# Kernel optimization log

Measured on AMD Instinct MI355X. Metric: run time of the kernel, lower is better.

The kernel has to match this reference:

```python
import jax, jax.numpy as jnp
import numpy as np

EMB = 1024
N_HEAD = 16
D_QK = 128  # emb_dim // h_qk
D_V = 128   # emb_dim // h_v


def setup_inputs() -> dict:
    key = jax.random.key(0)
    ks = jax.random.split(key, 9)
    s_in = 1.0 / np.sqrt(EMB)
    s_pr = 1.0 / np.sqrt(N_HEAD * D_V)
    return {
        "X": jax.random.normal(ks[0], (2, 2048, EMB), dtype=jnp.float32),
        "Wq": jax.random.uniform(ks[1], (EMB, N_HEAD * D_QK), jnp.float32, -s_in, s_in),
        "bq": jax.random.uniform(ks[2], (N_HEAD * D_QK,), jnp.float32, -s_in, s_in),
        "Wk": jax.random.uniform(ks[3], (EMB, N_HEAD * D_QK), jnp.float32, -s_in, s_in),
        "bk": jax.random.uniform(ks[4], (N_HEAD * D_QK,), jnp.float32, -s_in, s_in),
        "Wv": jax.random.uniform(ks[5], (EMB, N_HEAD * D_V), jnp.float32, -s_in, s_in),
        "bv": jax.random.uniform(ks[6], (N_HEAD * D_V,), jnp.float32, -s_in, s_in),
        "Wp": jax.random.uniform(ks[7], (N_HEAD * D_V, EMB), jnp.float32, -s_pr, s_pr),
        "bp": jax.random.uniform(ks[8], (EMB,), jnp.float32, -s_pr, s_pr),
    }


def reference(X, Wq, bq, Wk, bk, Wv, bv, Wp, bp):
    b, t, d = X.shape
    # projections -> (b, h, t, dh)
    Q = (X @ Wq + bq).reshape(b, t, N_HEAD, D_QK).transpose(0, 2, 1, 3)
    K = (X @ Wk + bk).reshape(b, t, N_HEAD, D_QK).transpose(0, 2, 1, 3)
    V = (X @ Wv + bv).reshape(b, t, N_HEAD, D_V).transpose(0, 2, 1, 3)
    scale = 1.0 / jnp.sqrt(jnp.asarray(D_QK, X.dtype))
    att = jnp.einsum("bhqd,bhkd->bhqk", Q, K) * scale  # (b,h,t,t)
    causal = jnp.tril(jnp.ones((t, t), dtype=bool))
    att = jnp.where(causal[None, None], att, jnp.asarray(-jnp.inf, att.dtype))
    att = jax.nn.softmax(att, axis=-1)
    y = jnp.einsum("bhqk,bhkd->bhqd", att, V)
    y = y.transpose(0, 2, 1, 3).reshape(b, t, N_HEAD * D_V)
    return y @ Wp + bp
```

## Files before the change

kernel.cpp:

```cpp
#include <hip/hip_runtime.h>
#include <hip/hip_bf16.h>
#include <math.h>

#define EMB   1024
#define NHEAD 16
#define DHEAD 128
#define TSEQ  2048
#define NB    2
#define MROWS (NB * TSEQ)
#define QKVN  (NHEAD * DHEAD)

typedef __bf16 bf16x8 __attribute__((ext_vector_type(8)));
typedef __bf16 bf16x4 __attribute__((ext_vector_type(4)));
typedef float  f32x4  __attribute__((ext_vector_type(4)));

__device__ __forceinline__ unsigned pk_bf16(float a, float b) {
  union { __bf16 h; unsigned short u; } ca, cb;
  ca.h = (__bf16)a; cb.h = (__bf16)b;
  return (unsigned)ca.u | ((unsigned)cb.u << 16);
}

__global__ __launch_bounds__(256) void prep(
    const float* __restrict__ X,
    const float* __restrict__ Wq, const float* __restrict__ Wk,
    const float* __restrict__ Wv, const float* __restrict__ Wp,
    __bf16* __restrict__ Xb, __bf16* __restrict__ Wqt, __bf16* __restrict__ Wkt,
    __bf16* __restrict__ Wvt, __bf16* __restrict__ Wpt) {
  const int z = blockIdx.z;
  if (z == 4) {
    size_t id = ((size_t)(blockIdx.y * 64 + blockIdx.x)) * 2048 + threadIdx.x * 8;
    float4 v0 = *(const float4*)(X + id);
    float4 v1 = *(const float4*)(X + id + 4);
    bf16x8 o = {(__bf16)v0.x, (__bf16)v0.y, (__bf16)v0.z, (__bf16)v0.w,
                (__bf16)v1.x, (__bf16)v1.y, (__bf16)v1.z, (__bf16)v1.w};
    *(bf16x8*)(Xb + id) = o;
    return;
  }
  __shared__ __bf16 tile[32][33];
  const float* in; __bf16* out; int K_, N_, k0, n0;
  if (z < 3) {
    in = z == 0 ? Wq : z == 1 ? Wk : Wv;
    out = z == 0 ? Wqt : z == 1 ? Wkt : Wvt;
    K_ = EMB; N_ = QKVN; k0 = blockIdx.y * 32; n0 = blockIdx.x * 32;
  } else {
    in = Wp; out = Wpt; K_ = QKVN; N_ = EMB; k0 = blockIdx.x * 32; n0 = blockIdx.y * 32;
  }
  const int c = threadIdx.x & 31, r = threadIdx.x >> 5;
#pragma unroll
  for (int i = 0; i < 4; ++i) {
    int kk = r + i * 8;
    tile[kk][c] = (__bf16)in[(size_t)(k0 + kk) * N_ + n0 + c];
  }
  __syncthreads();
#pragma unroll
  for (int i = 0; i < 4; ++i) {
    int nn = r + i * 8;
    out[(size_t)(n0 + nn) * K_ + k0 + c] = tile[c][nn];
  }
}

template <int TM, int MODE, typename OT>
__device__ __forceinline__ void gemm_core(
    const __bf16* __restrict__ A, const __bf16* __restrict__ Bt,
    const float* __restrict__ bias, OT* __restrict__ C,
    int N, int K, int brow, int bcol, float osc,
    __bf16* As, __bf16* Bs) {
  const int tid = threadIdx.x;
  const int wv = tid >> 6, ln = tid & 63;
  const int cl = ln & 15, gp = ln >> 4;
  constexpr int SJ = (TM == 128) ? 4 : 2;
  const int rbase = (TM == 128) ? (wv >> 1) * 64 : 0;
  const int cbase = (TM == 128) ? (wv & 1) * 64 : wv * 32;

  f32x4 acc[4][SJ];
#pragma unroll
  for (int i = 0; i < 4; ++i)
#pragma unroll
    for (int j = 0; j < SJ; ++j) acc[i][j] = (f32x4){0.f, 0.f, 0.f, 0.f};

  for (int k0 = 0; k0 < K; k0 += 64) {
#pragma unroll
    for (int i = 0; i < TM / 32; ++i) {
      int idx = i * 256 + tid;
      int r = idx >> 3, cp = idx & 7, c = cp ^ (r & 7);
      __builtin_amdgcn_global_load_lds(
          (const __attribute__((address_space(1))) unsigned int*)(A + (size_t)(brow + r) * K + k0 + c * 8),
          (__attribute__((address_space(3))) unsigned int*)(As + (size_t)(i * 256 + wv * 64) * 8),
          16, 0, 0);
    }
#pragma unroll
    for (int i = 0; i < 4; ++i) {
      int idx = i * 256 + tid;
      int r = idx >> 3, cp = idx & 7, c = cp ^ (r & 7);
      __builtin_amdgcn_global_load_lds(
          (const __attribute__((address_space(1))) unsigned int*)(Bt + (size_t)(bcol + r) * K + k0 + c * 8),
          (__attribute__((address_space(3))) unsigned int*)(Bs + (size_t)(i * 256 + wv * 64) * 8),
          16, 0, 0);
    }
    __syncthreads();

#pragma unroll
    for (int kc = 0; kc < 2; ++kc) {
      bf16x8 af[4], bfr[SJ];
#pragma unroll
      for (int i = 0; i < 4; ++i) {
        int r = rbase + i * 16 + cl;
        int c = kc * 4 + gp;
        af[i] = *(const bf16x8*)(As + ((size_t)(r * 8 + (c ^ (r & 7)))) * 8);
      }
#pragma unroll
      for (int j = 0; j < SJ; ++j) {
        int r = cbase + j * 16 + cl;
        int c = kc * 4 + gp;
        bfr[j] = *(const bf16x8*)(Bs + ((size_t)(r * 8 + (c ^ (r & 7)))) * 8);
      }
#pragma unroll
      for (int i = 0; i < 4; ++i)
#pragma unroll
        for (int j = 0; j < SJ; ++j)
          acc[i][j] = __builtin_amdgcn_mfma_f32_16x16x32_bf16(af[i], bfr[j], acc[i][j], 0, 0, 0);
    }
    __syncthreads();
  }

#pragma unroll
  for (int j = 0; j < SJ; ++j) {
    int col = bcol + cbase + j * 16 + cl;
    float bb = bias[col];
    int h = col >> 7, d = col & 127;
#pragma unroll
    for (int i = 0; i < 4; ++i) {
      int row0 = brow + rbase + i * 16 + gp * 4;
#pragma unroll
      for (int rr = 0; rr < 4; ++rr) {
        float val = (acc[i][j][rr] + bb) * osc;
        if constexpr (MODE == 3) {
          C[(size_t)(row0 + rr) * N + col] = val;
        } else {
          int row = row0 + rr;
          int b = row >> 11, tok = row & 2047;
          int bh = b * NHEAD + h;
          size_t idx;
          if constexpr (MODE == 0) {
            idx = (((size_t)bh * 64 + (tok >> 5)) * 8 + ((tok >> 4) & 1) * 4 + (d >> 5)) * 512
                + (((d >> 3) & 3) * 16 + (tok & 15)) * 8 + (d & 7);
          } else if constexpr (MODE == 1) {
            idx = (((size_t)bh * 32 + (tok >> 6)) * 16 + ((tok >> 4) & 3) * 4 + (d >> 5)) * 512
                + (((d >> 3) & 3) * 16 + (tok & 15)) * 8 + (d & 7);
          } else {
            idx = (((size_t)bh * 32 + (tok >> 6)) * 16 + (d >> 4) * 2 + ((tok >> 5) & 1)) * 512
                + (((tok >> 3) & 3) * 16 + (d & 15)) * 8 + (tok & 7);
          }
          ((__bf16*)C)[idx] = (__bf16)val;
        }
      }
    }
  }
}

__global__ __launch_bounds__(256) void gemm_qkv(
    const __bf16* __restrict__ A,
    const __bf16* __restrict__ Wqt, const __bf16* __restrict__ Wkt, const __bf16* __restrict__ Wvt,
    const float* __restrict__ bq, const float* __restrict__ bk, const float* __restrict__ bv,
    __bf16* __restrict__ Qblk, __bf16* __restrict__ Kblk, __bf16* __restrict__ Vblk) {
  __shared__ __bf16 As[8192], Bs[8192];
  const int z = blockIdx.z;
  if (z == 0) {
    gemm_core<128, 0, __bf16>(A, Wqt, bq, Qblk, QKVN, EMB, blockIdx.y * 128, blockIdx.x * 128,
                              0.08838834764831845f, As, Bs);
  } else if (z == 1) {
    gemm_core<128, 1, __bf16>(A, Wkt, bk, Kblk, QKVN, EMB, blockIdx.y * 128, blockIdx.x * 128,
                              1.0f, As, Bs);
  } else {
    gemm_core<128, 2, __bf16>(A, Wvt, bv, Vblk, QKVN, EMB, blockIdx.y * 128, blockIdx.x * 128,
                              1.0f, As, Bs);
  }
}

__global__ __launch_bounds__(256) void gemm_proj(
    const __bf16* __restrict__ A, const __bf16* __restrict__ Bt,
    const float* __restrict__ bias, float* __restrict__ C) {
  __shared__ __bf16 As[4096], Bs[8192];
  gemm_core<64, 3, float>(A, Bt, bias, C, EMB, QKVN, blockIdx.y * 64, blockIdx.x * 128,
                          1.0f, As, Bs);
}

__global__ __launch_bounds__(64) void attn_mfma(
    const __bf16* __restrict__ Qblk, const __bf16* __restrict__ Kblk,
    const __bf16* __restrict__ Vblk, __bf16* __restrict__ Y) {
  const int ln = threadIdx.x;
  const int cl = ln & 15, gp = ln >> 4;

  const int x = blockIdx.x;
  const int bh = x & 31;
  const int qt = 63 - (x >> 5);
  const int b = bh >> 4, h = bh & 15;
  const int ntiles = (qt >> 1) + 1;
  const int qloc = qt * 32;
  const size_t grow = (size_t)b * TSEQ + qloc;

  bf16x8 qa[2][4];
  const __bf16* qb = Qblk + (((size_t)bh * 64 + qt) * 8) * 512 + ln * 8;
#pragma unroll
  for (int i = 0; i < 2; ++i)
#pragma unroll
    for (int kc = 0; kc < 4; ++kc)
      qa[i][kc] = *(const bf16x8*)(qb + (i * 4 + kc) * 512);

  f32x4 o[2][8];
#pragma unroll
  for (int i = 0; i < 2; ++i)
#pragma unroll
    for (int n = 0; n < 8; ++n) o[i][n] = (f32x4){0.f, 0.f, 0.f, 0.f};
  float l[2] = {0.f, 0.f};

  const int m0 = 32 * (gp & 1) + cl;
  const int m1 = m0 + 16;
  const bool hi = gp >= 2;

  for (int kt = 0; kt < ntiles; ++kt) {
    const __bf16* kb = Kblk + (((size_t)bh * 32 + kt) * 16) * 512 + ln * 8;
    const __bf16* vb = Vblk + (((size_t)bh * 32 + kt) * 16) * 512 + ln * 8;

    f32x4 sacc[2][4];
#pragma unroll
    for (int i = 0; i < 2; ++i)
#pragma unroll
      for (int s = 0; s < 4; ++s) sacc[i][s] = (f32x4){0.f, 0.f, 0.f, 0.f};
#pragma unroll
    for (int s = 0; s < 4; ++s) {
      bf16x8 kfr[4];
#pragma unroll
      for (int kc = 0; kc < 4; ++kc)
        kfr[kc] = *(const bf16x8*)(kb + (s * 4 + kc) * 512);
#pragma unroll
      for (int kc = 0; kc < 4; ++kc) {
        sacc[0][s] = __builtin_amdgcn_mfma_f32_16x16x32_bf16(kfr[kc], qa[0][kc], sacc[0][s], 0, 0, 0);
        sacc[1][s] = __builtin_amdgcn_mfma_f32_16x16x32_bf16(kfr[kc], qa[1][kc], sacc[1][s], 0, 0, 0);
      }
    }
    const bool diag = (kt * 64 + 63 > qloc);
    unsigned pk[2][4][2];
#pragma unroll
    for (int i = 0; i < 2; ++i) {
      float psum = 0.f;
      int q = qloc + i * 16 + cl;
#pragma unroll
      for (int s = 0; s < 4; ++s) {
        float e[4];
#pragma unroll
        for (int rg = 0; rg < 4; ++rg) {
          e[rg] = __expf(sacc[i][s][rg]);
          if (diag && (kt * 64 + s * 16 + gp * 4 + rg) > q) e[rg] = 0.f;
          psum += e[rg];
        }
        pk[i][s][0] = pk_bf16(e[0], e[1]);
        pk[i][s][1] = pk_bf16(e[2], e[3]);
      }
      psum += __shfl_xor(psum, 16, 64);
      psum += __shfl_xor(psum, 32, 64);
      l[i] += psum;
    }
#pragma unroll
    for (int k2 = 0; k2 < 2; ++k2) {
      bf16x8 vfr[8];
#pragma unroll
      for (int ds = 0; ds < 8; ++ds)
        vfr[ds] = *(const bf16x8*)(vb + (ds * 2 + k2) * 512);
      union PU { unsigned u[4]; bf16x8 v; } pf[2];
#pragma unroll
      for (int i = 0; i < 2; ++i) {
        unsigned a0 = __shfl(pk[i][2 * k2][0], m0, 64);
        unsigned b0 = __shfl(pk[i][2 * k2 + 1][0], m0, 64);
        unsigned a1 = __shfl(pk[i][2 * k2][1], m0, 64);
        unsigned b1 = __shfl(pk[i][2 * k2 + 1][1], m0, 64);
        unsigned a2 = __shfl(pk[i][2 * k2][0], m1, 64);
        unsigned b2 = __shfl(pk[i][2 * k2 + 1][0], m1, 64);
        unsigned a3 = __shfl(pk[i][2 * k2][1], m1, 64);
        unsigned b3 = __shfl(pk[i][2 * k2 + 1][1], m1, 64);
        pf[i].u[0] = hi ? b0 : a0;
        pf[i].u[1] = hi ? b1 : a1;
        pf[i].u[2] = hi ? b2 : a2;
        pf[i].u[3] = hi ? b3 : a3;
      }
#pragma unroll
      for (int ds = 0; ds < 8; ++ds) {
        o[0][ds] = __builtin_amdgcn_mfma_f32_16x16x32_bf16(vfr[ds], pf[0].v, o[0][ds], 0, 0, 0);
        o[1][ds] = __builtin_amdgcn_mfma_f32_16x16x32_bf16(vfr[ds], pf[1].v, o[1][ds], 0, 0, 0);
      }
    }
  }

#pragma unroll
  for (int i = 0; i < 2; ++i) {
    float inv = 1.0f / l[i];
    __bf16* yrow = Y + (grow + i * 16 + cl) * QKVN + h * DHEAD;
#pragma unroll
    for (int ds = 0; ds < 8; ++ds) {
      bf16x4 st = {(__bf16)(o[i][ds][0] * inv), (__bf16)(o[i][ds][1] * inv),
                   (__bf16)(o[i][ds][2] * inv), (__bf16)(o[i][ds][3] * inv)};
      *(bf16x4*)(yrow + ds * 16 + gp * 4) = st;
    }
  }
}

extern "C" void kernel_launch(void* const* d_in, const int* in_sizes, int n_in,
                              void* d_out, int out_size, void* d_ws, size_t ws_size,
                              hipStream_t stream) {
  const float* X  = (const float*)d_in[0];
  const float* Wq = (const float*)d_in[1];
  const float* bq = (const float*)d_in[2];
  const float* Wk = (const float*)d_in[3];
  const float* bk = (const float*)d_in[4];
  const float* Wv = (const float*)d_in[5];
  const float* bv = (const float*)d_in[6];
  const float* Wp = (const float*)d_in[7];
  const float* bp = (const float*)d_in[8];
  float* out = (float*)d_out;

  const size_t xsz = (size_t)MROWS * EMB;
  const size_t wsz = (size_t)EMB * QKVN;
  const size_t msz = (size_t)MROWS * QKVN;
  __bf16* Xb   = (__bf16*)d_ws;
  __bf16* Wqt  = Xb + xsz;
  __bf16* Wkt  = Wqt + wsz;
  __bf16* Wvt  = Wkt + wsz;
  __bf16* Wpt  = Wvt + wsz;
  __bf16* Qblk = Wpt + wsz;
  __bf16* Kblk = Qblk + msz;
  __bf16* Vblk = Kblk + msz;
  __bf16* Yb   = Vblk + msz;

  dim3 blk(256);

  prep<<<dim3(64, 32, 5), blk, 0, stream>>>(X, Wq, Wk, Wv, Wp, Xb, Wqt, Wkt, Wvt, Wpt);

  gemm_qkv<<<dim3(QKVN / 128, MROWS / 128, 3), blk, 0, stream>>>(
      Xb, Wqt, Wkt, Wvt, bq, bk, bv, Qblk, Kblk, Vblk);

  attn_mfma<<<dim3(2048), dim3(64), 0, stream>>>(Qblk, Kblk, Vblk, Yb);

  gemm_proj<<<dim3(EMB / 128, MROWS / 64), blk, 0, stream>>>(Yb, Wpt, bp, out);
}
```

Measured before the change: 303.4 us.

## Split long causal attention rows across KV chunks with atomic fp32 accumulation

Query tiles with long causal KV ranges are split into chunks of up to 8 KV tiles, so 5120 single-wave blocks run instead of 2048 with uneven work. Partial unnormalised outputs and row sums are accumulated with fp32 atomics into a zeroed workspace. A new kernel then normalises them and writes bf16 Y; short rows still write Y directly. This trades the original load imbalance and tail for a large memset, heavy atomic traffic and an extra kernel launch. It is only correct if the partial softmax uses a shared fixed offset rather than a per-block running max.

Measured after the change: 481.9 us. 58.8% more time.

```diff
diff --git a/kernel.cpp b/kernel.cpp
--- a/kernel.cpp
+++ b/kernel.cpp
@@ -185,19 +185,27 @@
                           1.0f, As, Bs);
 }
 
-__global__ __launch_bounds__(64) void attn_mfma(
+__global__ __launch_bounds__(64) void attn_part(
     const __bf16* __restrict__ Qblk, const __bf16* __restrict__ Kblk,
-    const __bf16* __restrict__ Vblk, __bf16* __restrict__ Y) {
+    const __bf16* __restrict__ Vblk, __bf16* __restrict__ Y,
+    float* __restrict__ Oacc, float* __restrict__ Lacc) {
   const int ln = threadIdx.x;
   const int cl = ln & 15, gp = ln >> 4;
 
   const int x = blockIdx.x;
   const int bh = x & 31;
-  const int qt = 63 - (x >> 5);
+  const int w = x >> 5;
+  int qt, c;
+  if (w < 64)       { qt = 48 + (w >> 2); c = w & 3; }
+  else if (w < 112) { int u = w - 64; int q3 = u / 3; qt = 32 + q3; c = u - 3 * q3; }
+  else if (w < 144) { int u = w - 112; qt = 16 + (u >> 1); c = u & 1; }
+  else              { qt = w - 144; c = 0; }
+  const int nt = (qt >> 1) + 1;
+  const int t0 = c * 8;
+  const int t1 = (t0 + 8 < nt) ? (t0 + 8) : nt;
+
   const int b = bh >> 4, h = bh & 15;
-  const int ntiles = (qt >> 1) + 1;
   const int qloc = qt * 32;
-  const size_t grow = (size_t)b * TSEQ + qloc;
 
   bf16x8 qa[2][4];
   const __bf16* qb = Qblk + (((size_t)bh * 64 + qt) * 8) * 512 + ln * 8;
@@ -218,7 +226,7 @@
   const int m1 = m0 + 16;
   const bool hi = gp >= 2;
 
-  for (int kt = 0; kt < ntiles; ++kt) {
+  for (int kt = t0; kt < t1; ++kt) {
     const __bf16* kb = Kblk + (((size_t)bh * 32 + kt) * 16) * 512 + ln * 8;
     const __bf16* vb = Vblk + (((size_t)bh * 32 + kt) * 16) * 512 + ln * 8;
 
@@ -291,16 +299,58 @@
     }
   }
 
-#pragma unroll
-  for (int i = 0; i < 2; ++i) {
-    float inv = 1.0f / l[i];
-    __bf16* yrow = Y + (grow + i * 16 + cl) * QKVN + h * DHEAD;
-#pragma unroll
-    for (int ds = 0; ds < 8; ++ds) {
-      bf16x4 st = {(__bf16)(o[i][ds][0] * inv), (__bf16)(o[i][ds][1] * inv),
-                   (__bf16)(o[i][ds][2] * inv), (__bf16)(o[i][ds][3] * inv)};
-      *(bf16x4*)(yrow + ds * 16 + gp * 4) = st;
-    }
+  if (qt < 16) {
+#pragma unroll
+    for (int i = 0; i < 2; ++i) {
+      float inv = 1.0f / l[i];
+      __bf16* yrow = Y + ((size_t)(b * TSEQ + qloc + i * 16 + cl)) * QKVN + h * DHEAD;
+#pragma unroll
+      for (int ds = 0; ds < 8; ++ds) {
+        bf16x4 st = {(__bf16)(o[i][ds][0] * inv), (__bf16)(o[i][ds][1] * inv),
+                     (__bf16)(o[i][ds][2] * inv), (__bf16)(o[i][ds][3] * inv)};
+        *(bf16x4*)(yrow + ds * 16 + gp * 4) = st;
+      }
+    }
+  } else {
+    const size_t obase = (((size_t)bh * 64 + qt) * 32) * 128;
+#pragma unroll
+    for (int i = 0; i < 2; ++i) {
+      float* orow = Oacc + obase + (size_t)(i * 16 + cl) * 128 + gp * 4;
+#pragma unroll
+      for (int ds = 0; ds < 8; ++ds)
+#pragma unroll
+        for (int rg = 0; rg < 4; ++rg)
+          unsafeAtomicAdd(orow + ds * 16 + rg, o[i][ds][rg]);
+    }
+    if (ln < 16) {
+#pragma unroll
+      for (int i = 0; i < 2; ++i)
+        unsafeAtomicAdd(Lacc + ((size_t)bh * 64 + qt) * 32 + i * 16 + ln, l[i]);
+    }
+  }
+}
+
+__global__ __launch_bounds__(256) void attn_norm(
+    const float* __restrict__ Oacc, const float* __restrict__ Lacc,
+    __bf16* __restrict__ Y) {
+  const int bid = blockIdx.x;
+  const int bh = bid & 31;
+  const int qt = 16 + (bid >> 5);
+  const int b = bh >> 4, h = bh & 15;
+  const int q = threadIdx.x >> 3;
+  const int dc = threadIdx.x & 7;
+  const float inv = 1.0f / Lacc[((size_t)bh * 64 + qt) * 32 + q];
+  const float* op = Oacc + ((((size_t)bh * 64 + qt) * 32 + q) * 128) + dc * 16;
+  __bf16* yp = Y + ((size_t)(b * TSEQ + qt * 32 + q)) * QKVN + h * DHEAD + dc * 16;
+#pragma unroll
+  for (int half = 0; half < 2; ++half) {
+    f32x4 v0 = *(const f32x4*)(op + half * 8);
+    f32x4 v1 = *(const f32x4*)(op + half * 8 + 4);
+    bf16x8 st = {(__bf16)(v0[0] * inv), (__bf16)(v0[1] * inv),
+                 (__bf16)(v0[2] * inv), (__bf16)(v0[3] * inv),
+                 (__bf16)(v1[0] * inv), (__bf16)(v1[1] * inv),
+                 (__bf16)(v1[2] * inv), (__bf16)(v1[3] * inv)};
+    *(bf16x8*)(yp + half * 8) = st;
   }
 }
 
@@ -330,15 +380,21 @@
   __bf16* Kblk = Qblk + msz;
   __bf16* Vblk = Kblk + msz;
   __bf16* Yb   = Vblk + msz;
+  float*  Oacc = (float*)(Yb + msz);
+  float*  Lacc = Oacc + (size_t)32 * 64 * 32 * 128;
 
   dim3 blk(256);
+
+  hipMemsetAsync(Oacc, 0, ((size_t)32 * 64 * 32 * 128 + 65536) * sizeof(float), stream);
 
   prep<<<dim3(64, 32, 5), blk, 0, stream>>>(X, Wq, Wk, Wv, Wp, Xb, Wqt, Wkt, Wvt, Wpt);
 
   gemm_qkv<<<dim3(QKVN / 128, MROWS / 128, 3), blk, 0, stream>>>(
       Xb, Wqt, Wkt, Wvt, bq, bk, bv, Qblk, Kblk, Vblk);
 
-  attn_mfma<<<dim3(2048), dim3(64), 0, stream>>>(Qblk, Kblk, Vblk, Yb);
+  attn_part<<<dim3(5120), dim3(64), 0, stream>>>(Qblk, Kblk, Vblk, Yb, Oacc, Lacc);
+
+  attn_norm<<<dim3(1536), blk, 0, stream>>>(Oacc, Lacc, Yb);
 
   gemm_proj<<<dim3(EMB / 128, MROWS / 64), blk, 0, stream>>>(Yb, Wpt, bp, out);
 }
```
